# Performance work log

Hardware: AMD Instinct MI355X
Metric: run time of the kernel (lower is better)

The kernel has to match this reference:

```python
import jax, jax.numpy as jnp
import numpy as np

B, T, D, H = 2, 4096, 512, 8
HD = D // H

def setup_inputs() -> dict:
    key = jax.random.key(0)
    ks = jax.random.split(key, 5)
    x = jax.random.normal(ks[0], (B, T, D), dtype=jnp.float32)
    # causal mask: masked_fill where mask == 0
    mask = jnp.tril(jnp.ones((T, T), dtype=jnp.int32))[None, None, :, :]
    qkv_w = jax.random.normal(ks[1], (D, 3 * D), dtype=jnp.float32) * (D ** -0.5)
    qkv_b = jax.random.normal(ks[2], (3 * D,), dtype=jnp.float32) * 0.02
    proj_w = jax.random.normal(ks[3], (D, D), dtype=jnp.float32) * (D ** -0.5)
    proj_b = jax.random.normal(ks[4], (D,), dtype=jnp.float32) * 0.02
    return {"x": x, "mask": mask, "qkv_w": qkv_w, "qkv_b": qkv_b,
            "proj_w": proj_w, "proj_b": proj_b}

def reference(x, mask, qkv_w, qkv_b, proj_w, proj_b):
    b, t, c = x.shape
    qkv = x @ qkv_w + qkv_b                      # [B,T,3D]
    q, k, v = jnp.split(qkv, 3, axis=-1)
    # [B,T,D] -> [B,H,T,hd]
    def heads(a):
        return a.reshape(b, t, H, HD).transpose(0, 2, 1, 3)
    q, k, v = heads(q), heads(k), heads(v)
    att = jnp.einsum('bhqd,bhkd->bhqk', q, k) / (HD ** 0.5)
    att = jnp.where(mask == 0, -jnp.inf, att)
    att = jax.nn.softmax(att, axis=-1)           # dropout p=0.0 -> identity
    out = jnp.einsum('bhqk,bhkd->bhqd', att, v)  # [B,H,T,hd]
    out = out.transpose(0, 2, 1, 3).reshape(b, t, c)
    return out @ proj_w + proj_b
```

## Files before the change

kernel.cpp:

```cpp
#include <hip/hip_runtime.h>
#include <hip/hip_bf16.h>


typedef __attribute__((ext_vector_type(8))) short bf16x8;
typedef __attribute__((ext_vector_type(4))) float f32x4;
typedef __attribute__((ext_vector_type(16))) float f32x16;
typedef __attribute__((ext_vector_type(2))) int i32x2;

#define DEV static __device__ __forceinline__

DEV unsigned short f2bf(float f) {
    union { float f; unsigned u; } a; a.f = f;
    unsigned r = a.u + 0x7FFFu + ((a.u >> 16) & 1u);
    return (unsigned short)(r >> 16);
}

DEV unsigned pack2(float a, float b) {
    unsigned r;
    asm("v_cvt_pk_bf16_f32 %0, %1, %2" : "=v"(r) : "v"(a), "v"(b));
    return r;
}

DEV void glds16(const void* g, void* l) {
    __builtin_amdgcn_global_load_lds(
        (const __attribute__((address_space(1))) void*)g,
        (__attribute__((address_space(3))) void*)l,
        16, 0, 0);
}

DEV f32x4 mfma(bf16x8 a, bf16x8 b, f32x4 c) {
    return __builtin_amdgcn_mfma_f32_16x16x32_bf16(a, b, c, 0, 0, 0);
}

DEV f32x16 mfma32(bf16x8 a, bf16x8 b, f32x16 c) {
    return __builtin_amdgcn_mfma_f32_32x32x16_bf16(a, b, c, 0, 0, 0);
}

DEV void plswap(unsigned& a, unsigned& b) {
#if __has_builtin(__builtin_amdgcn_permlane32_swap)
    i32x2 r = __builtin_amdgcn_permlane32_swap((int)a, (int)b, false, false);
    a = (unsigned)r.x; b = (unsigned)r.y;
#else
    unsigned sa = __shfl_xor(a, 32), sb = __shfl_xor(b, 32);
    bool hi = (threadIdx.x & 32) != 0;
    unsigned na = hi ? sb : a;
    unsigned nb = hi ? b : sa;
    a = na; b = nb;
#endif
}

DEV float xhalf_sum(float x) {
    unsigned a = __float_as_uint(x), b = a;
    plswap(a, b);
    return __uint_as_float(a) + __uint_as_float(b);
}

__global__ __launch_bounds__(256) void k_prep(const float* __restrict__ x,
                                              unsigned short* __restrict__ xb,
                                              const float* __restrict__ qkv_w,
                                              unsigned short* __restrict__ wqkvT,
                                              const float* __restrict__ proj_w,
                                              unsigned short* __restrict__ wprojT) {
    const int tid = threadIdx.x;
    int id = blockIdx.x;
    if (id < 2048) {
        const int n4 = 8192 * 512 / 4;
        for (int i = id * 256 + tid; i < n4; i += 2048 * 256) {
            float4 v = ((const float4*)x)[i];
            ushort4 o;
            o.x = f2bf(v.x); o.y = f2bf(v.y); o.z = f2bf(v.z); o.w = f2bf(v.w);
            ((ushort4*)xb)[i] = o;
        }
        return;
    }
    id -= 2048;
    __shared__ float t[64][65];
    const float* src; unsigned short* dst; int R, C, bx, by;
    if (id < 192) { src = qkv_w; dst = wqkvT; R = 512; C = 1536; bx = id % 24; by = id / 24; }
    else { id -= 192; src = proj_w; dst = wprojT; R = 512; C = 512; bx = id & 7; by = id >> 3; }
#pragma unroll
    for (int e = 0; e < 16; ++e) {
        int idx = e * 256 + tid;
        int r = idx >> 6, c = idx & 63;
        t[r][c] = src[(by * 64 + r) * C + bx * 64 + c];
    }
    __syncthreads();
#pragma unroll
    for (int e = 0; e < 16; ++e) {
        int idx = e * 256 + tid;
        int r = idx >> 6, c = idx & 63;
        dst[(bx * 64 + r) * R + by * 64 + c] = f2bf(t[c][r]);
    }
}

__global__ __launch_bounds__(256) void k_gemm_qkv(
    const unsigned short* __restrict__ xb, const unsigned short* __restrict__ wT,
    const float* __restrict__ bias,
    unsigned short* __restrict__ Qb, unsigned short* __restrict__ Kb,
    unsigned short* __restrict__ Vtb)
{
    __shared__ __attribute__((aligned(16))) char smem[65536];
    char* lA0 = smem;          char* lB0 = smem + 16384;
    char* lA1 = smem + 32768;  char* lB1 = smem + 49152;
    const int tid = threadIdx.x, lane = tid & 63, w = tid >> 6;
    const int qi = lane & 15, g = lane >> 4;
    const int bm = blockIdx.x & 63, bn = blockIdx.x >> 6;
    const int m0 = bm * 128, n0 = bn * 128;
    const int wr = w >> 1, wc = w & 1;
    const int srow = lane >> 3, sch = (lane & 7) ^ srow;
    const int swz = (qi & 7) << 4;
    f32x4 zero = {0.f, 0.f, 0.f, 0.f};
    f32x4 acc[4][4];
#pragma unroll
    for (int i = 0; i < 4; ++i)
#pragma unroll
        for (int j = 0; j < 4; ++j) acc[i][j] = zero;

#pragma unroll
    for (int i = 0; i < 4; ++i) {
        int c = w * 4 + i;
        int row = c * 8 + srow;
        glds16(xb + (m0 + row) * 512 + sch * 8, lA0 + c * 1024);
        glds16(wT + (n0 + row) * 512 + sch * 8, lB0 + c * 1024);
    }

    for (int kt = 0; kt < 8; ++kt) {
        const int cur = kt & 1;
        if (kt + 1 < 8) {
            char* ad = cur ? lA0 : lA1;
            char* bd = cur ? lB0 : lB1;
#pragma unroll
            for (int i = 0; i < 4; ++i) {
                int c = w * 4 + i;
                int row = c * 8 + srow;
                glds16(xb + (m0 + row) * 512 + (kt + 1) * 64 + sch * 8, ad + c * 1024);
                glds16(wT + (n0 + row) * 512 + (kt + 1) * 64 + sch * 8, bd + c * 1024);
            }
            asm volatile("s_waitcnt vmcnt(8)" ::: "memory");
        } else {
            asm volatile("s_waitcnt vmcnt(0)" ::: "memory");
        }
        __builtin_amdgcn_s_barrier();
        __builtin_amdgcn_sched_barrier(0);

        const char* la = cur ? lA1 : lA0;
        const char* lb = cur ? lB1 : lB0;
#pragma unroll
        for (int k2 = 0; k2 < 2; ++k2) {
            bf16x8 af[4], bfr[4];
#pragma unroll
            for (int i = 0; i < 4; ++i) {
                int ra = wr * 64 + i * 16 + qi;
                af[i] = *(const bf16x8*)(la + ra * 128 + ((k2 * 64 + g * 16) ^ swz));
                int rb = wc * 64 + i * 16 + qi;
                bfr[i] = *(const bf16x8*)(lb + rb * 128 + ((k2 * 64 + g * 16) ^ swz));
            }
#pragma unroll
            for (int mi = 0; mi < 4; ++mi)
#pragma unroll
                for (int ni = 0; ni < 4; ++ni)
                    acc[mi][ni] = mfma(af[mi], bfr[ni], acc[mi][ni]);
        }
        __builtin_amdgcn_s_barrier();
        __builtin_amdgcn_sched_barrier(0);
    }

    const int comp = n0 >> 9;
#pragma unroll
    for (int mi = 0; mi < 4; ++mi) {
        int mbase = m0 + wr * 64 + mi * 16 + g * 4;
        int b = mbase >> 12, t = mbase & 4095;
#pragma unroll
        for (int ni = 0; ni < 4; ++ni) {
            int n = n0 + wc * 64 + ni * 16 + qi;
            float bn = bias[n];
            int nn = n & 511;
            int h = nn >> 6, d = nn & 63;
            if (comp == 0) {
                unsigned short* dst = Qb + ((b * 8 + h) * 4096 + t) * 64 + d;
#pragma unroll
                for (int r = 0; r < 4; ++r)
                    dst[r * 64] = f2bf((acc[mi][ni][r] + bn) * 0.18033688011112042f);
            } else if (comp == 1) {
                unsigned short* dst = Kb + ((b * 8 + h) * 4096 + t) * 64 + d;
#pragma unroll
                for (int r = 0; r < 4; ++r)
                    dst[r * 64] = f2bf(acc[mi][ni][r] + bn);
            } else {
                ushort4 pk4;
                pk4.x = f2bf(acc[mi][ni][0] + bn);
                pk4.y = f2bf(acc[mi][ni][1] + bn);
                pk4.z = f2bf(acc[mi][ni][2] + bn);
                pk4.w = f2bf(acc[mi][ni][3] + bn);
                *(ushort4*)(Vtb + ((b * 8 + h) * 64 + d) * 4096 + t) = pk4;
            }
        }
    }
}

__global__ __launch_bounds__(512) void k_attn(
    const unsigned short* __restrict__ Qb, const unsigned short* __restrict__ Kb,
    const unsigned short* __restrict__ Vtb, unsigned short* __restrict__ Ob)
{
    __shared__ __attribute__((aligned(16))) char smem[65536];
    const int tid = threadIdx.x, lane = tid & 63, w = tid >> 6;
    const int l31 = lane & 31, l7 = lane & 7, h = lane >> 5;
    const int pr = w >> 1, sub = w & 1;
    const int idx = blockIdx.x;
    const int bh = idx & 15;
    const int p = idx >> 4;
    const unsigned short* Qh = Qb + bh * 4096 * 64;
    const unsigned short* Kh = Kb + bh * 4096 * 64;
    const unsigned short* Vh = Vtb + bh * 4096 * 64;
    const float NEGINF = -__builtin_inff();

    char* myK = smem + pr * 16384;
    char* myV = myK + 8192;

    const int srw = lane >> 3;
    const int sxor = (l7 ^ srw) * 8;
    const int kOffE = (sub * 32 + srw) * 64 + sxor;
    const int vOffE = (sub * 32 + srw) * 4096 + sxor;
    const int ldsO = sub * 4096;

    const int rowbase = l31 * 128;
    int cx[4];
#pragma unroll
    for (int c = 0; c < 4; ++c) cx[c] = ((2 * c + h) ^ l7) * 16;

    const int qrel = (sub << 5) + l31;

    f32x16 z16;
#pragma unroll
    for (int r = 0; r < 16; ++r) z16[r] = 0.f;

    for (int si = 0; si < 2; ++si) {
        const int qt = si ? p : 63 - p;
        const int Tmax = (qt >> 2) + 1;
        const int qrow = qt * 64 + sub * 32 + l31;

        bf16x8 qf[4];
#pragma unroll
        for (int c = 0; c < 4; ++c)
            qf[c] = *(const bf16x8*)(Qh + qrow * 64 + 16 * c + 8 * h);

        f32x16 o0 = z16, o1 = z16;
        float li = 0.f;

        for (int t = 0; t < Tmax; ++t) {
            const int j = 4 * t + pr;
            const bool act = (j <= qt);
            if (act) {
                const unsigned short* kp = Kh + j * 4096 + kOffE;
                const unsigned short* vp = Vh + vOffE + j * 64;
#pragma unroll
                for (int i = 0; i < 4; ++i) {
                    glds16(kp + i * 512,   myK + ldsO + i * 1024);
                    glds16(vp + i * 32768, myV + ldsO + i * 1024);
                }
            }
            __syncthreads();
            if (act) {
                const char* lk = myK;
                const char* lv = myV;
                f32x16 s0, s1;
                __builtin_amdgcn_s_setprio(1);
                {
                    bf16x8 k0 = *(const bf16x8*)(lk + rowbase + cx[0]);
                    bf16x8 k1 = *(const bf16x8*)(lk + 4096 + rowbase + cx[0]);
                    s0 = mfma32(k0, qf[0], z16);
                    s1 = mfma32(k1, qf[0], z16);
                }
#pragma unroll
                for (int c = 1; c < 4; ++c) {
                    bf16x8 k0 = *(const bf16x8*)(lk + rowbase + cx[c]);
                    bf16x8 k1 = *(const bf16x8*)(lk + 4096 + rowbase + cx[c]);
                    s0 = mfma32(k0, qf[c], s0);
                    s1 = mfma32(k1, qf[c], s1);
                }
                __builtin_amdgcn_s_setprio(0);

                if (j == qt) {
#pragma unroll
                    for (int r = 0; r < 16; ++r) {
                        int rr = 4 * h + (r & 3) + 8 * (r >> 2);
                        if (rr > qrel) s0[r] = NEGINF;
                        if (rr + 32 > qrel) s1[r] = NEGINF;
                    }
                }

#pragma unroll
                for (int r = 0; r < 16; ++r) {
                    s0[r] = __builtin_amdgcn_exp2f(s0[r]);
                    s1[r] = __builtin_amdgcn_exp2f(s1[r]);
                }
                float a8[8];
#pragma unroll
                for (int r = 0; r < 8; ++r)
                    a8[r] = (s0[r] + s0[r + 8]) + (s1[r] + s1[r + 8]);
                float b0 = (a8[0] + a8[4]) + (a8[1] + a8[5]);
                float b1 = (a8[2] + a8[6]) + (a8[3] + a8[7]);
                li += xhalf_sum(b0 + b1);

                __builtin_amdgcn_s_setprio(1);
#pragma unroll
                for (int c2 = 0; c2 < 4; ++c2) {
                    unsigned u0w, u1w, u2w, u3w;
                    if (c2 < 2) {
                        const int b0i = 8 * c2;
                        u0w = pack2(s0[b0i + 0], s0[b0i + 1]);
                        u1w = pack2(s0[b0i + 2], s0[b0i + 3]);
                        u2w = pack2(s0[b0i + 4], s0[b0i + 5]);
                        u3w = pack2(s0[b0i + 6], s0[b0i + 7]);
                    } else {
                        const int b0i = 8 * (c2 - 2);
                        u0w = pack2(s1[b0i + 0], s1[b0i + 1]);
                        u1w = pack2(s1[b0i + 2], s1[b0i + 3]);
                        u2w = pack2(s1[b0i + 4], s1[b0i + 5]);
                        u3w = pack2(s1[b0i + 6], s1[b0i + 7]);
                    }
                    plswap(u0w, u2w);
                    plswap(u1w, u3w);
                    union { unsigned u[4]; bf16x8 v; } pf;
                    pf.u[0] = u0w; pf.u[1] = u1w; pf.u[2] = u2w; pf.u[3] = u3w;
                    bf16x8 v0 = *(const bf16x8*)(lv + rowbase + cx[c2]);
                    bf16x8 v1 = *(const bf16x8*)(lv + 4096 + rowbase + cx[c2]);
                    o0 = mfma32(v0, pf.v, o0);
                    o1 = mfma32(v1, pf.v, o1);
                }
                __builtin_amdgcn_s_setprio(0);
            }
            __syncthreads();
        }

        float* fsm = (float*)smem;
        if (pr != 0) {
            float* slot = fsm + ((((pr - 1) << 1) + sub) * 64 + lane) * 36;
#pragma unroll
            for (int r4 = 0; r4 < 4; ++r4) {
                f32x4 v0 = {o0[4 * r4], o0[4 * r4 + 1], o0[4 * r4 + 2], o0[4 * r4 + 3]};
                f32x4 v1 = {o1[4 * r4], o1[4 * r4 + 1], o1[4 * r4 + 2], o1[4 * r4 + 3]};
                *(f32x4*)(slot + 4 * r4) = v0;
                *(f32x4*)(slot + 16 + 4 * r4) = v1;
            }
            slot[32] = li;
        }
        __syncthreads();
        if (pr == 0) {
            float l = li;
#pragma unroll
            for (int i = 0; i < 3; ++i) {
                const float* s = fsm + (((i << 1) + sub) * 64 + lane) * 36;
                l += s[32];
#pragma unroll
                for (int r4 = 0; r4 < 4; ++r4) {
                    f32x4 a = *(const f32x4*)(s + 4 * r4);
                    f32x4 b = *(const f32x4*)(s + 16 + 4 * r4);
#pragma unroll
                    for (int e = 0; e < 4; ++e) {
                        o0[4 * r4 + e] += a[e];
                        o1[4 * r4 + e] += b[e];
                    }
                }
            }
            float inv = 1.f / l;
            unsigned short* orow = Ob + ((bh >> 3) * 4096 + qrow) * 512 + (bh & 7) * 64 + 4 * h;
#pragma unroll
            for (int g2 = 0; g2 < 4; ++g2) {
                union { ushort4 s4; unsigned u[2]; } a;
                a.u[0] = pack2(o0[4 * g2 + 0] * inv, o0[4 * g2 + 1] * inv);
                a.u[1] = pack2(o0[4 * g2 + 2] * inv, o0[4 * g2 + 3] * inv);
                *(ushort4*)(orow + 8 * g2) = a.s4;
                a.u[0] = pack2(o1[4 * g2 + 0] * inv, o1[4 * g2 + 1] * inv);
                a.u[1] = pack2(o1[4 * g2 + 2] * inv, o1[4 * g2 + 3] * inv);
                *(ushort4*)(orow + 32 + 8 * g2) = a.s4;
            }
        }
        __syncthreads();
    }
}

__global__ __launch_bounds__(256) void k_gemm_proj(
    const unsigned short* __restrict__ Ob, const unsigned short* __restrict__ wT,
    const float* __restrict__ bias, float* __restrict__ out)
{
    __shared__ __attribute__((aligned(16))) char smem[65536];
    char* lA0 = smem;          char* lB0 = smem + 16384;
    char* lA1 = smem + 32768;  char* lB1 = smem + 49152;
    const int tid = threadIdx.x, lane = tid & 63, w = tid >> 6;
    const int qi = lane & 15, g = lane >> 4;
    const int bm = blockIdx.x & 63, bn = blockIdx.x >> 6;
    const int m0 = bm * 128, n0 = bn * 128;
    const int wr = w >> 1, wc = w & 1;
    const int srow = lane >> 3, sch = (lane & 7) ^ srow;
    const int swz = (qi & 7) << 4;
    f32x4 zero = {0.f, 0.f, 0.f, 0.f};
    f32x4 acc[4][4];
#pragma unroll
    for (int i = 0; i < 4; ++i)
#pragma unroll
        for (int j = 0; j < 4; ++j) acc[i][j] = zero;

#pragma unroll
    for (int i = 0; i < 4; ++i) {
        int c = w * 4 + i;
        int row = c * 8 + srow;
        glds16(Ob + (m0 + row) * 512 + sch * 8, lA0 + c * 1024);
        glds16(wT + (n0 + row) * 512 + sch * 8, lB0 + c * 1024);
    }

    for (int kt = 0; kt < 8; ++kt) {
        const int cur = kt & 1;
        if (kt + 1 < 8) {
            char* ad = cur ? lA0 : lA1;
            char* bd = cur ? lB0 : lB1;
#pragma unroll
            for (int i = 0; i < 4; ++i) {
                int c = w * 4 + i;
                int row = c * 8 + srow;
                glds16(Ob + (m0 + row) * 512 + (kt + 1) * 64 + sch * 8, ad + c * 1024);
                glds16(wT + (n0 + row) * 512 + (kt + 1) * 64 + sch * 8, bd + c * 1024);
            }
            asm volatile("s_waitcnt vmcnt(8)" ::: "memory");
        } else {
            asm volatile("s_waitcnt vmcnt(0)" ::: "memory");
        }
        __builtin_amdgcn_s_barrier();
        __builtin_amdgcn_sched_barrier(0);

        const char* la = cur ? lA1 : lA0;
        const char* lb = cur ? lB1 : lB0;
#pragma unroll
        for (int k2 = 0; k2 < 2; ++k2) {
            bf16x8 af[4], bfr[4];
#pragma unroll
            for (int i = 0; i < 4; ++i) {
                int ra = wr * 64 + i * 16 + qi;
                af[i] = *(const bf16x8*)(la + ra * 128 + ((k2 * 64 + g * 16) ^ swz));
                int rb = wc * 64 + i * 16 + qi;
                bfr[i] = *(const bf16x8*)(lb + rb * 128 + ((k2 * 64 + g * 16) ^ swz));
            }
#pragma unroll
            for (int mi = 0; mi < 4; ++mi)
#pragma unroll
                for (int ni = 0; ni < 4; ++ni)
                    acc[mi][ni] = mfma(af[mi], bfr[ni], acc[mi][ni]);
        }
        __builtin_amdgcn_s_barrier();
        __builtin_amdgcn_sched_barrier(0);
    }

    float bn4[4];
#pragma unroll
    for (int ni = 0; ni < 4; ++ni) bn4[ni] = bias[n0 + wc * 64 + ni * 16 + qi];

    float* st = (float*)smem;
#pragma unroll
    for (int cc = 0; cc < 4; ++cc) {
        __syncthreads();
        if (wr == (cc >> 1)) {
            const int mi0 = (cc & 1) * 2;
#pragma unroll
            for (int mm = 0; mm < 2; ++mm) {
                int mi = mi0 + mm;
                int rr0 = mi * 16 + g * 4 - (cc & 1) * 32;
#pragma unroll
                for (int ni = 0; ni < 4; ++ni) {
                    int col = wc * 64 + ni * 16 + qi;
#pragma unroll
                    for (int r = 0; r < 4; ++r)
                        st[(rr0 + r) * 132 + col] = acc[mi][ni][r] + bn4[ni];
                }
            }
        }
        __syncthreads();
#pragma unroll
        for (int e = 0; e < 4; ++e) {
            int fid = e * 256 + tid;
            int row = fid >> 5, c4 = fid & 31;
            f32x4 v = *(const f32x4*)(st + row * 132 + 4 * c4);
            *(f32x4*)(out + (m0 + cc * 32 + row) * 512 + n0 + 4 * c4) = v;
        }
    }
}

extern "C" void kernel_launch(void* const* d_in, const int* in_sizes, int n_in,
                              void* d_out, int out_size, void* d_ws, size_t ws_size,
                              hipStream_t stream) {
    const float* x      = (const float*)d_in[0];
    const float* qkv_w  = (const float*)d_in[2];
    const float* qkv_b  = (const float*)d_in[3];
    const float* proj_w = (const float*)d_in[4];
    const float* proj_b = (const float*)d_in[5];

    char* ws = (char*)d_ws;
    unsigned short* xb     = (unsigned short*)(ws);
    unsigned short* wqkvT  = (unsigned short*)(ws +  8388608);
    unsigned short* wprojT = (unsigned short*)(ws +  9961472);
    unsigned short* Qb     = (unsigned short*)(ws + 10485760);
    unsigned short* Kb     = (unsigned short*)(ws + 18874368);
    unsigned short* Vtb    = (unsigned short*)(ws + 27262976);
    unsigned short* Ob     = (unsigned short*)(ws + 35651584);
    float* out = (float*)d_out;

    k_prep<<<2304, 256, 0, stream>>>(x, xb, qkv_w, wqkvT, proj_w, wprojT);
    k_gemm_qkv<<<768, 256, 0, stream>>>(xb, wqkvT, qkv_b, Qb, Kb, Vtb);
    k_attn<<<512, 512, 0, stream>>>(Qb, Kb, Vtb, Ob);
    k_gemm_proj<<<256, 256, 0, stream>>>(Ob, wprojT, proj_b, out);
}
```

Baseline: 93.48 us.

## Double-buffer 32-key K/V tiles in LDS and skip masked half-tiles per wave

Each wave pair now handles 32-key tiles instead of 64-key tiles. The next tile is prefetched into a second LDS buffer while the current one is computed, with explicit vmcnt waits and raw barriers in place of __syncthreads. The causal work bound is computed per sub-wave, so waves whose 32 query rows lie fully below the diagonal skip the fully masked half-tile, and the V layout and swizzle are changed to match. This aims to hide global-to-LDS latency and remove wasted masked MFMA work, at the cost of twice as many loop iterations and barriers and more delicate wait-count handling.

```diff
diff --git a/kernel.cpp b/kernel.cpp
--- a/kernel.cpp
+++ b/kernel.cpp
@@ -214,21 +214,21 @@
     const unsigned short* Vh = Vtb + bh * 4096 * 64;
     const float NEGINF = -__builtin_inff();
 
-    char* myK = smem + pr * 16384;
-    char* myV = myK + 8192;
+    char* base = smem + pr * 16384;
 
     const int srw = lane >> 3;
-    const int sxor = (l7 ^ srw) * 8;
-    const int kOffE = (sub * 32 + srw) * 64 + sxor;
-    const int vOffE = (sub * 32 + srw) * 4096 + sxor;
-    const int ldsO = sub * 4096;
-
-    const int rowbase = l31 * 128;
-    int cx[4];
+    const int kOffE = (sub * 16 + srw) * 64 + (l7 ^ srw) * 8;
+    const int vOffE = (sub * 32 + (lane >> 2)) * 4096
+                    + ((lane & 3) ^ ((lane >> 3) & 3)) * 8;
+    const int ldsO = sub * 2048;
+
+    const int rowK = l31 * 128;
+    const int rowV = l31 * 64;
+    int cx[4], cxv[2];
 #pragma unroll
     for (int c = 0; c < 4; ++c) cx[c] = ((2 * c + h) ^ l7) * 16;
-
-    const int qrel = (sub << 5) + l31;
+#pragma unroll
+    for (int c = 0; c < 2; ++c) cxv[c] = ((2 * c + h) ^ ((l31 >> 1) & 3)) * 16;
 
     f32x16 z16;
 #pragma unroll
@@ -236,7 +236,10 @@
 
     for (int si = 0; si < 2; ++si) {
         const int qt = si ? p : 63 - p;
-        const int Tmax = (qt >> 2) + 1;
+        const int jmaxw = 2 * qt + sub;
+        const int myT = (jmaxw >= pr) ? ((jmaxw - pr) >> 2) + 1 : 0;
+        const int prT = (2 * qt + 1 >= pr) ? ((2 * qt + 1 - pr) >> 2) + 1 : 0;
+        const int Tmax = ((2 * qt + 1) >> 2) + 1;
         const int qrow = qt * 64 + sub * 32 + l31;
 
         bf16x8 qf[4];
@@ -247,93 +250,88 @@
         f32x16 o0 = z16, o1 = z16;
         float li = 0.f;
 
+        if (prT > 0) {
+            const unsigned short* kp = Kh + pr * 2048 + kOffE;
+            const unsigned short* vp = Vh + vOffE + pr * 32;
+#pragma unroll
+            for (int i = 0; i < 2; ++i) {
+                glds16(kp + i * 512,   base + ldsO + i * 1024);
+                glds16(vp + i * 65536, base + 4096 + ldsO + i * 1024);
+            }
+        }
+
         for (int t = 0; t < Tmax; ++t) {
-            const int j = 4 * t + pr;
-            const bool act = (j <= qt);
-            if (act) {
-                const unsigned short* kp = Kh + j * 4096 + kOffE;
-                const unsigned short* vp = Vh + vOffE + j * 64;
-#pragma unroll
-                for (int i = 0; i < 4; ++i) {
-                    glds16(kp + i * 512,   myK + ldsO + i * 1024);
-                    glds16(vp + i * 32768, myV + ldsO + i * 1024);
+            const int cur = t & 1;
+            if (t + 1 < prT) {
+                const int jn = 4 * (t + 1) + pr;
+                const unsigned short* kp = Kh + jn * 2048 + kOffE;
+                const unsigned short* vp = Vh + vOffE + jn * 32;
+                char* dst = base + (cur ? 0 : 8192);
+#pragma unroll
+                for (int i = 0; i < 2; ++i) {
+                    glds16(kp + i * 512,   dst + ldsO + i * 1024);
+                    glds16(vp + i * 65536, dst + 4096 + ldsO + i * 1024);
                 }
-            }
-            __syncthreads();
-            if (act) {
-                const char* lk = myK;
-                const char* lv = myV;
-                f32x16 s0, s1;
+                asm volatile("s_waitcnt vmcnt(4)" ::: "memory");
+            } else {
+                asm volatile("s_waitcnt vmcnt(0)" ::: "memory");
+            }
+            __builtin_amdgcn_s_barrier();
+            __builtin_amdgcn_sched_barrier(0);
+
+            if (t < myT) {
+                const int j = 4 * t + pr;
+                const char* lk = base + (cur ? 8192 : 0);
+                const char* lv = lk + 4096;
+                f32x16 s;
                 __builtin_amdgcn_s_setprio(1);
-                {
-                    bf16x8 k0 = *(const bf16x8*)(lk + rowbase + cx[0]);
-                    bf16x8 k1 = *(const bf16x8*)(lk + 4096 + rowbase + cx[0]);
-                    s0 = mfma32(k0, qf[0], z16);
-                    s1 = mfma32(k1, qf[0], z16);
-                }
-#pragma unroll
-                for (int c = 1; c < 4; ++c) {
-                    bf16x8 k0 = *(const bf16x8*)(lk + rowbase + cx[c]);
-                    bf16x8 k1 = *(const bf16x8*)(lk + 4096 + rowbase + cx[c]);
-                    s0 = mfma32(k0, qf[c], s0);
-                    s1 = mfma32(k1, qf[c], s1);
-                }
+                s = mfma32(*(const bf16x8*)(lk + rowK + cx[0]), qf[0], z16);
+#pragma unroll
+                for (int c = 1; c < 4; ++c)
+                    s = mfma32(*(const bf16x8*)(lk + rowK + cx[c]), qf[c], s);
                 __builtin_amdgcn_s_setprio(0);
 
-                if (j == qt) {
+                if (j == jmaxw) {
 #pragma unroll
                     for (int r = 0; r < 16; ++r) {
                         int rr = 4 * h + (r & 3) + 8 * (r >> 2);
-                        if (rr > qrel) s0[r] = NEGINF;
-                        if (rr + 32 > qrel) s1[r] = NEGINF;
+                        if (rr > l31) s[r] = NEGINF;
                     }
                 }
 
 #pragma unroll
-                for (int r = 0; r < 16; ++r) {
-                    s0[r] = __builtin_amdgcn_exp2f(s0[r]);
-                    s1[r] = __builtin_amdgcn_exp2f(s1[r]);
-                }
-                float a8[8];
-#pragma unroll
-                for (int r = 0; r < 8; ++r)
-                    a8[r] = (s0[r] + s0[r + 8]) + (s1[r] + s1[r + 8]);
-                float b0 = (a8[0] + a8[4]) + (a8[1] + a8[5]);
-                float b1 = (a8[2] + a8[6]) + (a8[3] + a8[7]);
-                li += xhalf_sum(b0 + b1);
+                for (int r = 0; r < 16; ++r) s[r] = __builtin_amdgcn_exp2f(s[r]);
+                float a4[4];
+#pragma unroll
+                for (int r = 0; r < 4; ++r)
+                    a4[r] = (s[r] + s[r + 4]) + (s[r + 8] + s[r + 12]);
+                li += xhalf_sum((a4[0] + a4[1]) + (a4[2] + a4[3]));
 
                 __builtin_amdgcn_s_setprio(1);
 #pragma unroll
-                for (int c2 = 0; c2 < 4; ++c2) {
-                    unsigned u0w, u1w, u2w, u3w;
-                    if (c2 < 2) {
-                        const int b0i = 8 * c2;
-                        u0w = pack2(s0[b0i + 0], s0[b0i + 1]);
-                        u1w = pack2(s0[b0i + 2], s0[b0i + 3]);
-                        u2w = pack2(s0[b0i + 4], s0[b0i + 5]);
-                        u3w = pack2(s0[b0i + 6], s0[b0i + 7]);
-                    } else {
-                        const int b0i = 8 * (c2 - 2);
-                        u0w = pack2(s1[b0i + 0], s1[b0i + 1]);
-                        u1w = pack2(s1[b0i + 2], s1[b0i + 3]);
-                        u2w = pack2(s1[b0i + 4], s1[b0i + 5]);
-                        u3w = pack2(s1[b0i + 6], s1[b0i + 7]);
-                    }
+                for (int c2 = 0; c2 < 2; ++c2) {
+                    const int b0i = 8 * c2;
+                    unsigned u0w = pack2(s[b0i + 0], s[b0i + 1]);
+                    unsigned u1w = pack2(s[b0i + 2], s[b0i + 3]);
+                    unsigned u2w = pack2(s[b0i + 4], s[b0i + 5]);
+                    unsigned u3w = pack2(s[b0i + 6], s[b0i + 7]);
                     plswap(u0w, u2w);
                     plswap(u1w, u3w);
                     union { unsigned u[4]; bf16x8 v; } pf;
                     pf.u[0] = u0w; pf.u[1] = u1w; pf.u[2] = u2w; pf.u[3] = u3w;
-                    bf16x8 v0 = *(const bf16x8*)(lv + rowbase + cx[c2]);
-                    bf16x8 v1 = *(const bf16x8*)(lv + 4096 + rowbase + cx[c2]);
+                    bf16x8 v0 = *(const bf16x8*)(lv + rowV + cxv[c2]);
+                    bf16x8 v1 = *(const bf16x8*)(lv + 2048 + rowV + cxv[c2]);
                     o0 = mfma32(v0, pf.v, o0);
                     o1 = mfma32(v1, pf.v, o1);
                 }
                 __builtin_amdgcn_s_setprio(0);
             }
-            __syncthreads();
+            __builtin_amdgcn_s_barrier();
+            __builtin_amdgcn_sched_barrier(0);
         }
 
         float* fsm = (float*)smem;
+        __syncthreads();
         if (pr != 0) {
             float* slot = fsm + ((((pr - 1) << 1) + sub) * 64 + lane) * 36;
 #pragma unroll
```

New measurement: 97.40 us. 1.04x slower.
